# Performance work log

Measured on AMD Instinct MI355X. Metric: run time of the kernel, lower is better.

## Reference

```python
import jax, jax.numpy as jnp
import numpy as np

G, S, P = 128, 32, 16          # graphs, subgraphs per graph, nodes per subgraph
D, C, NH, OUT = 768, 256, 4, 7 # input dim, hidden dim, GAT heads, classes


def setup_inputs() -> dict:
    key = jax.random.key(0)
    ks = jax.random.split(key, 17)
    n = lambda k, shape, s=0.05: jax.random.normal(k, shape, dtype=jnp.float32) * s
    return {
        "x": jax.random.normal(ks[0], (G, S, P, D), dtype=jnp.float32),
        # GATConv(768 -> 256, heads=4, concat=False): lin weight, att vectors, bias
        "gat_W": n(ks[1], (D, NH * C)),
        "att_src": n(ks[2], (NH, C)),
        "att_dst": n(ks[3], (NH, C)),
        "gat_b": n(ks[4], (C,)),
        # GRU(256 -> 256), torch layout [3*H, in]
        "gru_Wih": n(ks[5], (3 * C, C)),
        "gru_Whh": n(ks[6], (3 * C, C)),
        "gru_bih": n(ks[7], (3 * C,)),
        "gru_bhh": n(ks[8], (3 * C,)),
        # scale_up_projection Linear(256 -> 768)
        "up_W": n(ks[9], (D, C)),
        "up_b": n(ks[10], (D,)),
        # speaker_projection Linear(1536 -> 768) + ReLU
        "sp_W": n(ks[11], (D, 2 * D)),
        "sp_b": n(ks[12], (D,)),
        # GlobalAttention gate Linear(256 -> 1)
        "att_W": n(ks[13], (1, C)),
        "att_b": n(ks[14], (1,)),
        # classifier Linear(256 -> 7)
        "cls_W": n(ks[15], (OUT, C)),
        "cls_b": n(ks[16], (OUT,)),
    }


def _gat(x, W, a_src, a_dst, b):
    # PyG GATConv on a star graph (speaker = local node 0 -> all others) with
    # default add_self_loops=True, negative_slope=0.2, concat=False (mean over heads).
    # x: [G, P, D]
    h = jnp.einsum('gpd,dhc->gphc', x, W.reshape(D, NH, C))     # per-head transform
    es = jnp.sum(h * a_src, -1)                                 # [G, P, NH]
    ed = jnp.sum(h * a_dst, -1)
    lrelu = lambda v: jnp.where(v > 0, v, 0.2 * v)
    e_spk = lrelu(es[:, :1] + ed)   # edge speaker -> t
    e_slf = lrelu(es + ed)          # self loop t -> t
    w = jax.nn.softmax(jnp.stack([e_spk, e_slf], -1), axis=-1)  # [G, P, NH, 2]
    # for t == 0 both terms are h[:,0] and weights sum to 1, matching the
    # speaker node receiving only its self loop.
    out = w[..., 0:1] * h[:, :1] + w[..., 1:2] * h              # [G, P, NH, C]
    return out.mean(axis=2) + b


def _gru_cell(xin, h, Wih, Whh, bih, bhh):
    gi = xin @ Wih.T + bih
    gh = h @ Whh.T + bhh
    ir, iz, inn = jnp.split(gi, 3, -1)
    hr, hz, hn = jnp.split(gh, 3, -1)
    r = jax.nn.sigmoid(ir + hr)
    z = jax.nn.sigmoid(iz + hz)
    return (1 - z) * jnp.tanh(inn + r * hn) + z * h


def _forward(x, gat_W, att_src, att_dst, gat_b, gru_Wih, gru_Whh, gru_bih, gru_bhh,
             up_W, up_b, sp_W, sp_b, att_W, att_b, cls_W, cls_b):
    g, s, p, d = x.shape
    m0 = _gat(x[:, 0], gat_W, att_src, att_dst, gat_b)  # [G, P, C]
    h0 = jnp.zeros((g, p, C), x.dtype)

    def step(carry, _):
        h_run, m_prev = carry
        # running GRU hidden over memory prefix, then one zero-input step
        # (equivalent to rerunning the GRU over [m_0..m_{j-1}, 0])
        h_run = _gru_cell(m_prev, h_run, gru_Wih, gru_Whh, gru_bih, gru_bhh)
        h_nxt = _gru_cell(jnp.zeros_like(h_run), h_run, gru_Wih, gru_Whh, gru_bih, gru_bhh)
        pooled = h_nxt @ up_W.T + up_b                  # [G, P, D]
        # faithful to source: non_speaker_indices covers ALL nodes (torch.equal
        # shape-mismatch bug), and speaker_info is read AFTER the overwrite,
        # so the speaker concat is [pooled, pooled] and raw x[:, j>=1] is unused.
        spk = jnp.concatenate([pooled[:, 0], pooled[:, 0]], -1)  # [G, 2D]
        spk = jax.nn.relu(spk @ sp_W.T + sp_b)
        x_new = pooled.at[:, 0].set(spk)
        m = _gat(x_new, gat_W, att_src, att_dst, gat_b)
        return (h_run, m), m

    (_, _), ms = jax.lax.scan(step, (h0, m0), None, length=s - 1)
    mem = jnp.concatenate([m0[None], ms], axis=0)        # [S, G, P, C]
    # GlobalAttention pool over the P nodes of each subgraph memory state
    gate = jax.nn.softmax(jnp.squeeze(mem @ att_W.T + att_b, -1), axis=-1)  # [S, G, P]
    pooled = jnp.einsum('sgp,sgpc->sgc', gate, mem)
    logits = pooled @ cls_W.T + cls_b                    # [S, G, OUT]
    # torch stacks graph-major: [G*S, 1, OUT]
    return jnp.transpose(logits, (1, 0, 2)).reshape(g * s, 1, OUT)


def reference(x, gat_W, att_src, att_dst, gat_b, gru_Wih, gru_Whh, gru_bih, gru_bhh,
              up_W, up_b, sp_W, sp_b, att_W, att_b, cls_W, cls_b):
    return _forward(x, gat_W, att_src, att_dst, gat_b, gru_Wih, gru_Whh, gru_bih,
                    gru_bhh, up_W, up_b, sp_W, sp_b, att_W, att_b, cls_W, cls_b)
```

## Files before the change

### kernel.cpp

```cpp
#include <hip/hip_runtime.h>
#include <math.h>

#define NG 128
#define NS 32
#define NP 16
#define ND 768
#define NC 256
#define NHD 4
#define NOUT 7
#define NR 2048

typedef unsigned short ushortT;
typedef short bf16x8 __attribute__((ext_vector_type(8)));
typedef float f32x4 __attribute__((ext_vector_type(4)));

__device__ __forceinline__ ushortT f2b(float f) {
    union { float f; unsigned u; } v; v.f = f;
    unsigned r = (v.u + 0x7FFF + ((v.u >> 16) & 1)) >> 16;
    return (ushortT)r;
}
__device__ __forceinline__ float b2f(ushortT u) {
    union { unsigned u; float f; } v; v.u = ((unsigned)u) << 16; return v.f;
}
__device__ __forceinline__ float sigf(float v) { return 1.f / (1.f + expf(-v)); }

#define MFMA16(a, b, c) __builtin_amdgcn_mfma_f32_16x16x32_bf16((a), (b), (c), 0, 0, 0)

__global__ __launch_bounds__(512) void gru12spk_kernel(
    const ushortT* __restrict__ mB, const ushortT* __restrict__ hB,
    float* __restrict__ hF,
    const ushortT* __restrict__ WihB, const ushortT* __restrict__ WhhB,
    const ushortT* __restrict__ WusB,
    const float* __restrict__ bih, const float* __restrict__ bhh,
    const float* __restrict__ busv,
    ushortT* __restrict__ hBout, ushortT* __restrict__ hnB,
    ushortT* __restrict__ spkB)
{
    __shared__ short Am[16 * 264];
    __shared__ short Ah[16 * 264];
    __shared__ short Bs[768 * 40];
    const int g = blockIdx.x, tid = threadIdx.x;
    const int w = tid >> 6, lane = tid & 63;
    const int quad = lane >> 4, l15 = lane & 15;
    const int row0 = g * 16;

    {
        const int row = tid >> 5, kc = (tid & 31) * 8;
        *(uint4*)&Am[row * 264 + kc] = *(const uint4*)(mB + (size_t)(row0 + row) * NC + kc);
        *(uint4*)&Ah[row * 264 + kc] = *(const uint4*)(hB + (size_t)(row0 + row) * NC + kc);
    }

    f32x4 ai[3][2], ah[3][2];
#pragma unroll
    for (int gt = 0; gt < 3; ++gt)
#pragma unroll
        for (int nf = 0; nf < 2; ++nf) {
            ai[gt][nf] = (f32x4){0.f, 0.f, 0.f, 0.f};
            ah[gt][nf] = (f32x4){0.f, 0.f, 0.f, 0.f};
        }

    for (int kk = 0; kk < NC; kk += 32) {
        __syncthreads();
        for (int s = tid; s < 3072; s += 512) {
            const int row = s >> 2, kq = (s & 3) * 8;
            *(uint4*)&Bs[row * 40 + kq] = *(const uint4*)(WihB + (size_t)row * NC + kk + kq);
        }
        __syncthreads();
        bf16x8 af = *(const bf16x8*)&Am[l15 * 264 + kk + quad * 8];
#pragma unroll
        for (int gt = 0; gt < 3; ++gt)
#pragma unroll
            for (int nf = 0; nf < 2; ++nf) {
                bf16x8 bv = *(const bf16x8*)&Bs[(gt * 256 + w * 32 + nf * 16 + l15) * 40 + quad * 8];
                ai[gt][nf] = MFMA16(af, bv, ai[gt][nf]);
            }
    }
    for (int kk = 0; kk < NC; kk += 32) {
        __syncthreads();
        for (int s = tid; s < 3072; s += 512) {
            const int row = s >> 2, kq = (s & 3) * 8;
            *(uint4*)&Bs[row * 40 + kq] = *(const uint4*)(WhhB + (size_t)row * NC + kk + kq);
        }
        __syncthreads();
        bf16x8 af = *(const bf16x8*)&Ah[l15 * 264 + kk + quad * 8];
#pragma unroll
        for (int gt = 0; gt < 3; ++gt)
#pragma unroll
            for (int nf = 0; nf < 2; ++nf) {
                bf16x8 bv = *(const bf16x8*)&Bs[(gt * 256 + w * 32 + nf * 16 + l15) * 40 + quad * 8];
                ah[gt][nf] = MFMA16(af, bv, ah[gt][nf]);
            }
    }
    float hreg[2][4];
#pragma unroll
    for (int nf = 0; nf < 2; ++nf) {
        const int c = w * 32 + nf * 16 + l15;
        const float br = bih[c], bz = bih[256 + c], bn = bih[512 + c];
        const float cr = bhh[c], cz = bhh[256 + c], cn = bhh[512 + c];
#pragma unroll
        for (int r = 0; r < 4; ++r) {
            const int row = quad * 4 + r;
            const size_t idx = (size_t)(row0 + row) * NC + c;
            const float hold = hF[idx];
            const float rg = sigf(ai[0][nf][r] + br + ah[0][nf][r] + cr);
            const float zg = sigf(ai[1][nf][r] + bz + ah[1][nf][r] + cz);
            const float ng = tanhf(ai[2][nf][r] + bn + rg * (ah[2][nf][r] + cn));
            const float hn = (1.f - zg) * ng + zg * hold;
            hreg[nf][r] = hn;
            hF[idx] = hn;
            hBout[idx] = f2b(hn);
            Am[row * 264 + c] = (short)f2b(hn);
        }
    }
    f32x4 a2[3][2];
#pragma unroll
    for (int gt = 0; gt < 3; ++gt)
#pragma unroll
        for (int nf = 0; nf < 2; ++nf) a2[gt][nf] = (f32x4){0.f, 0.f, 0.f, 0.f};
    for (int kk = 0; kk < NC; kk += 32) {
        __syncthreads();
        for (int s = tid; s < 3072; s += 512) {
            const int row = s >> 2, kq = (s & 3) * 8;
            *(uint4*)&Bs[row * 40 + kq] = *(const uint4*)(WhhB + (size_t)row * NC + kk + kq);
        }
        __syncthreads();
        bf16x8 af = *(const bf16x8*)&Am[l15 * 264 + kk + quad * 8];
#pragma unroll
        for (int gt = 0; gt < 3; ++gt)
#pragma unroll
            for (int nf = 0; nf < 2; ++nf) {
                bf16x8 bv = *(const bf16x8*)&Bs[(gt * 256 + w * 32 + nf * 16 + l15) * 40 + quad * 8];
                a2[gt][nf] = MFMA16(af, bv, a2[gt][nf]);
            }
    }
#pragma unroll
    for (int nf = 0; nf < 2; ++nf) {
        const int c = w * 32 + nf * 16 + l15;
        const float br = bih[c], bz = bih[256 + c], bn = bih[512 + c];
        const float cr = bhh[c], cz = bhh[256 + c], cn = bhh[512 + c];
#pragma unroll
        for (int r = 0; r < 4; ++r) {
            const int row = quad * 4 + r;
            const size_t idx = (size_t)(row0 + row) * NC + c;
            const float rg = sigf(br + a2[0][nf][r] + cr);
            const float zg = sigf(bz + a2[1][nf][r] + cz);
            const float ng = tanhf(bn + rg * (a2[2][nf][r] + cn));
            const float hv = (1.f - zg) * ng + zg * hreg[nf][r];
            const ushortT hb16 = f2b(hv);
            hnB[idx] = hb16;
            Ah[row * 264 + c] = (short)hb16;
        }
    }
    __syncthreads();
    for (int o = tid; o < ND; o += 512) {
        float s = busv[o];
        const ushortT* wr = WusB + (size_t)o * NC;
#pragma unroll 8
        for (int k8 = 0; k8 < 32; ++k8) {
            bf16x8 hv8 = *(const bf16x8*)&Ah[k8 * 8];
            bf16x8 wv8 = *(const bf16x8*)(wr + k8 * 8);
#pragma unroll
            for (int i = 0; i < 8; ++i) s += b2f((ushortT)hv8[i]) * b2f((ushortT)wv8[i]);
        }
        spkB[(size_t)g * ND + o] = f2b(fmaxf(s, 0.f));
    }
}

__global__ __launch_bounds__(256) void gatovr_kernel(
    const ushortT* __restrict__ hnB, const ushortT* __restrict__ spkB,
    const ushortT* __restrict__ WcombB, const ushortT* __restrict__ gatB,
    const float* __restrict__ bcomb, float* __restrict__ hbuf)
{
    __shared__ short As[64 * 40];
    __shared__ short Bs[64 * 40];
    const int b = blockIdx.x, tid = threadIdx.x;
    const int lane = tid & 63, wid = tid >> 6;
    const int quad = lane >> 4, l15 = lane & 15;
    const int mh = (wid & 1) * 32, nh = (wid >> 1) * 32;
    const int sr = tid >> 2, skq = (tid & 3) * 8;

    const bool ovr = (b >= 512);
    int row0, col0, K;
    const ushortT *A, *Bt;
    if (!ovr) {
        row0 = (b >> 4) * 64; col0 = (b & 15) * 64;
        A = hnB; Bt = WcombB; K = NC;
    } else {
        const int t = b - 512;
        row0 = (t & 1) * 64; col0 = (t >> 1) * 64;
        A = spkB; Bt = gatB; K = ND;
    }
    const ushortT* aptr = A + (size_t)(row0 + sr) * K;
    const ushortT* bptr = Bt + (size_t)(col0 + sr) * K;

    f32x4 acc[2][2];
    for (int i = 0; i < 2; ++i)
        for (int j = 0; j < 2; ++j) acc[i][j] = (f32x4){0.f, 0.f, 0.f, 0.f};

    for (int kk = 0; kk < K; kk += 32) {
        __syncthreads();
        *(uint4*)&As[sr * 40 + skq] = *(const uint4*)(aptr + kk + skq);
        *(uint4*)&Bs[sr * 40 + skq] = *(const uint4*)(bptr + kk + skq);
        __syncthreads();
        bf16x8 af0 = *(const bf16x8*)&As[(mh + l15) * 40 + quad * 8];
        bf16x8 af1 = *(const bf16x8*)&As[(mh + 16 + l15) * 40 + quad * 8];
        bf16x8 bf0 = *(const bf16x8*)&Bs[(nh + l15) * 40 + quad * 8];
        bf16x8 bf1 = *(const bf16x8*)&Bs[(nh + 16 + l15) * 40 + quad * 8];
        acc[0][0] = MFMA16(af0, bf0, acc[0][0]);
        acc[0][1] = MFMA16(af0, bf1, acc[0][1]);
        acc[1][0] = MFMA16(af1, bf0, acc[1][0]);
        acc[1][1] = MFMA16(af1, bf1, acc[1][1]);
    }
#pragma unroll
    for (int mt = 0; mt < 2; ++mt)
#pragma unroll
        for (int nt = 0; nt < 2; ++nt) {
            const int gc = col0 + nh + nt * 16 + l15;
            const float bv = ovr ? 0.f : bcomb[gc];
#pragma unroll
            for (int r = 0; r < 4; ++r) {
                const int gr = row0 + mh + mt * 16 + quad * 4 + r;
                const float v = acc[mt][nt][r] + bv;
                if (ovr) {
                    hbuf[(size_t)(gr * 16) * (NHD * NC) + gc] = v;
                } else if (gr & 15) {
                    hbuf[(size_t)gr * (NHD * NC) + gc] = v;
                }
            }
        }
}

__global__ __launch_bounds__(256) void fin_kernel(
    const float* __restrict__ hbuf, const float* __restrict__ att_src,
    const float* __restrict__ att_dst, const float* __restrict__ gat_b,
    const float* __restrict__ attW, const float* __restrict__ attb,
    const float* __restrict__ clsW, const float* __restrict__ clsb,
    ushortT* __restrict__ mB, float* __restrict__ outp, int s)
{
    const int g = blockIdx.x, tid = threadIdx.x;
    const int lane = tid & 63, wid = tid >> 6;
    __shared__ float es_s[16][4], ed_s[16][4];
    __shared__ float m_s[16][260];
    __shared__ float gate_s[16];
    __shared__ float pooled_s[256];
    const float* hb = hbuf + (size_t)g * NP * (NHD * NC);

    for (int pi = 0; pi < 4; ++pi) {
        const int p = wid * 4 + pi;
        const float* row = hb + p * (NHD * NC);
        float ss[4] = {0.f, 0.f, 0.f, 0.f}, sd[4] = {0.f, 0.f, 0.f, 0.f};
#pragma unroll
        for (int i = 0; i < 16; ++i) {
            const int col = lane + 64 * i;
            const float v = row[col];
            ss[i >> 2] += v * att_src[col];
            sd[i >> 2] += v * att_dst[col];
        }
        for (int off = 32; off; off >>= 1)
#pragma unroll
            for (int h = 0; h < 4; ++h) {
                ss[h] += __shfl_down(ss[h], off);
                sd[h] += __shfl_down(sd[h], off);
            }
        if (lane == 0)
#pragma unroll
            for (int h = 0; h < 4; ++h) { es_s[p][h] = ss[h]; ed_s[p][h] = sd[h]; }
    }
    __syncthreads();
    {
        const int p = tid >> 4, cb = (tid & 15) * 16;
        float accv[16];
#pragma unroll
        for (int cj = 0; cj < 16; ++cj) accv[cj] = 0.f;
#pragma unroll
        for (int h = 0; h < 4; ++h) {
            float e1 = es_s[0][h] + ed_s[p][h]; e1 = e1 > 0.f ? e1 : 0.2f * e1;
            float e2 = es_s[p][h] + ed_s[p][h]; e2 = e2 > 0.f ? e2 : 0.2f * e2;
            const float mx = fmaxf(e1, e2);
            float w0 = expf(e1 - mx), w1 = expf(e2 - mx);
            const float inv = 1.f / (w0 + w1);
            w0 *= inv; w1 *= inv;
            const float* r0 = hb + h * NC + cb;
            const float* rp = hb + p * (NHD * NC) + h * NC + cb;
#pragma unroll
            for (int cj = 0; cj < 16; ++cj) accv[cj] += w0 * r0[cj] + w1 * rp[cj];
        }
#pragma unroll
        for (int cj = 0; cj < 16; ++cj) {
            const float v = accv[cj] * 0.25f + gat_b[cb + cj];
            m_s[p][cb + cj] = v;
            mB[(size_t)(g * NP + p) * NC + cb + cj] = f2b(v);
        }
    }
    __syncthreads();
    for (int pi = 0; pi < 4; ++pi) {
        const int p = wid * 4 + pi;
        float sg = 0.f;
#pragma unroll
        for (int i = 0; i < 4; ++i) { const int c = lane + 64 * i; sg += m_s[p][c] * attW[c]; }
        for (int off = 32; off; off >>= 1) sg += __shfl_down(sg, off);
        if (lane == 0) gate_s[p] = sg + attb[0];
    }
    __syncthreads();
    float mx = -1e30f;
#pragma unroll
    for (int p = 0; p < 16; ++p) mx = fmaxf(mx, gate_s[p]);
    float ge[16], ssum = 0.f;
#pragma unroll
    for (int p = 0; p < 16; ++p) { ge[p] = expf(gate_s[p] - mx); ssum += ge[p]; }
    const float inv = 1.f / ssum;
    {
        float pc = 0.f;
#pragma unroll
        for (int p = 0; p < 16; ++p) pc += ge[p] * m_s[p][tid];
        pooled_s[tid] = pc * inv;
    }
    __syncthreads();
    const int o = tid >> 5, l32 = tid & 31;
    if (o < NOUT) {
        float a = 0.f;
#pragma unroll
        for (int i = 0; i < 8; ++i) {
            const int c = l32 + 32 * i;
            a += pooled_s[c] * clsW[o * NC + c];
        }
        for (int off = 16; off; off >>= 1) a += __shfl_down(a, off);
        if (l32 == 0) outp[((size_t)g * NS + s) * NOUT + o] = a + clsb[o];
    }
}

__global__ __launch_bounds__(256) void bgemm_kernel(
    const ushortT* __restrict__ A, const ushortT* __restrict__ Bt,
    const float* __restrict__ bias, float* __restrict__ outF,
    ushortT* __restrict__ outH, int N, int K, int act)
{
    __shared__ short As[64 * 40];
    __shared__ short Bs[64 * 40];
    const int tid = threadIdx.x;
    const int lane = tid & 63, wid = tid >> 6;
    const int quad = lane >> 4, l15 = lane & 15;
    const int row0 = blockIdx.y * 64, col0 = blockIdx.x * 64;
    const int mh = (wid & 1) * 32, nh = (wid >> 1) * 32;
    const int sr = tid >> 2, skq = (tid & 3) * 8;
    const ushortT* aptr = A + (size_t)(row0 + sr) * K;
    const ushortT* bptr = Bt + (size_t)(col0 + sr) * K;

    f32x4 acc[2][2];
    for (int i = 0; i < 2; ++i)
        for (int j = 0; j < 2; ++j) acc[i][j] = (f32x4){0.f, 0.f, 0.f, 0.f};

    for (int kk = 0; kk < K; kk += 32) {
        __syncthreads();
        *(uint4*)&As[sr * 40 + skq] = *(const uint4*)(aptr + kk + skq);
        *(uint4*)&Bs[sr * 40 + skq] = *(const uint4*)(bptr + kk + skq);
        __syncthreads();
        bf16x8 af0 = *(const bf16x8*)&As[(mh + l15) * 40 + quad * 8];
        bf16x8 af1 = *(const bf16x8*)&As[(mh + 16 + l15) * 40 + quad * 8];
        bf16x8 bf0 = *(const bf16x8*)&Bs[(nh + l15) * 40 + quad * 8];
        bf16x8 bf1 = *(const bf16x8*)&Bs[(nh + 16 + l15) * 40 + quad * 8];
        acc[0][0] = MFMA16(af0, bf0, acc[0][0]);
        acc[0][1] = MFMA16(af0, bf1, acc[0][1]);
        acc[1][0] = MFMA16(af1, bf0, acc[1][0]);
        acc[1][1] = MFMA16(af1, bf1, acc[1][1]);
    }
#pragma unroll
    for (int mt = 0; mt < 2; ++mt)
#pragma unroll
        for (int nt = 0; nt < 2; ++nt) {
            const int gc = col0 + nh + nt * 16 + l15;
            const float bv = bias ? bias[gc] : 0.f;
#pragma unroll
            for (int r = 0; r < 4; ++r) {
                const int gr = row0 + mh + mt * 16 + quad * 4 + r;
                float v = acc[mt][nt][r] + bv;
                if (act) v = fmaxf(v, 0.f);
                if (outF) outF[(size_t)gr * N + gc] = v;
                if (outH) outH[(size_t)gr * N + gc] = f2b(v);
            }
        }
}

__global__ __launch_bounds__(256) void cast_kernel(const float* __restrict__ a,
                                                   ushortT* __restrict__ b, int n) {
    const int i = blockIdx.x * 256 + threadIdx.x;
    if (i < n) b[i] = f2b(a[i]);
}
__global__ __launch_bounds__(256) void gatT_kernel(const float* __restrict__ gW,
                                                   ushortT* __restrict__ gB) {
    const int idx = blockIdx.x * 256 + threadIdx.x;
    const int c = idx / ND, d = idx - c * ND;
    gB[idx] = f2b(gW[(size_t)d * (NHD * NC) + c]);
}
__global__ __launch_bounds__(256) void upwT_kernel(const float* __restrict__ upW,
                                                   ushortT* __restrict__ o) {
    const int idx = blockIdx.x * 256 + threadIdx.x;
    const int k = idx / ND, d = idx - k * ND;
    o[idx] = f2b(upW[(size_t)d * NC + k]);
}
__global__ __launch_bounds__(256) void bcomb_kernel(const float* __restrict__ gW,
                                                    const float* __restrict__ up_b,
                                                    float* __restrict__ bc) {
    const int c = blockIdx.x * 256 + threadIdx.x;
    if (c >= NHD * NC) return;
    float a = 0.f;
    for (int d = 0; d < ND; ++d) a += up_b[d] * gW[(size_t)d * (NHD * NC) + c];
    bc[c] = a;
}
__global__ __launch_bounds__(256) void spwc_kernel(const float* __restrict__ spW,
                                                   float* __restrict__ o) {
    const int idx = blockIdx.x * 256 + threadIdx.x;
    const int r = idx / ND, d = idx - r * ND;
    o[idx] = spW[(size_t)r * (2 * ND) + d] + spW[(size_t)r * (2 * ND) + ND + d];
}
__global__ __launch_bounds__(256) void wus_kernel(const float* __restrict__ spWc,
                                                  const float* __restrict__ upW,
                                                  ushortT* __restrict__ WusB) {
    const int c = threadIdx.x;
    const int o0 = blockIdx.x * 16;
    float acc[16];
#pragma unroll
    for (int i = 0; i < 16; ++i) acc[i] = 0.f;
    for (int d = 0; d < ND; ++d) {
        const float u = upW[(size_t)d * NC + c];
#pragma unroll
        for (int i = 0; i < 16; ++i) acc[i] += spWc[(size_t)(o0 + i) * ND + d] * u;
    }
#pragma unroll
    for (int i = 0; i < 16; ++i) WusB[(size_t)(o0 + i) * NC + c] = f2b(acc[i]);
}
__global__ __launch_bounds__(256) void bus_kernel(const float* __restrict__ spWc,
                                                  const float* __restrict__ up_b,
                                                  const float* __restrict__ sp_b,
                                                  float* __restrict__ bus) {
    const int o = blockIdx.x * 256 + threadIdx.x;
    if (o >= ND) return;
    float a = sp_b[o];
    const float* sr = spWc + (size_t)o * ND;
    for (int d = 0; d < ND; ++d) a += sr[d] * up_b[d];
    bus[o] = a;
}
__global__ __launch_bounds__(256) void x0_kernel(const float* __restrict__ x,
                                                 ushortT* __restrict__ xb) {
    const int idx = blockIdx.x * 256 + threadIdx.x;
    const int row = idx / ND, d = idx - row * ND;
    const int g = row >> 4, p = row & 15;
    xb[idx] = f2b(x[((size_t)g * (NS * NP) + p) * ND + d]);
}
__global__ __launch_bounds__(256) void zh_kernel(float* hF, ushortT* hB) {
    const int idx = blockIdx.x * 256 + threadIdx.x;
    hF[idx] = 0.f;
    hB[idx] = 0;
}

extern "C" void kernel_launch(void* const* d_in, const int* in_sizes, int n_in,
                              void* d_out, int out_size, void* d_ws, size_t ws_size,
                              hipStream_t stream) {
    (void)in_sizes; (void)n_in; (void)out_size; (void)ws_size;
    const float* x       = (const float*)d_in[0];
    const float* gat_W   = (const float*)d_in[1];
    const float* att_src = (const float*)d_in[2];
    const float* att_dst = (const float*)d_in[3];
    const float* gat_b   = (const float*)d_in[4];
    const float* gru_Wih = (const float*)d_in[5];
    const float* gru_Whh = (const float*)d_in[6];
    const float* gru_bih = (const float*)d_in[7];
    const float* gru_bhh = (const float*)d_in[8];
    const float* up_W    = (const float*)d_in[9];
    const float* up_b    = (const float*)d_in[10];
    const float* sp_W    = (const float*)d_in[11];
    const float* sp_b    = (const float*)d_in[12];
    const float* att_W   = (const float*)d_in[13];
    const float* att_b   = (const float*)d_in[14];
    const float* cls_W   = (const float*)d_in[15];
    const float* cls_b   = (const float*)d_in[16];
    float* outp = (float*)d_out;

    char* w = (char*)d_ws;
    ushortT* xb    = (ushortT*)w; w += (size_t)NR * ND * 2;
    ushortT* WihB  = (ushortT*)w; w += (size_t)(3 * NC) * NC * 2;
    ushortT* WhhB  = (ushortT*)w; w += (size_t)(3 * NC) * NC * 2;
    ushortT* gatB  = (ushortT*)w; w += (size_t)(NHD * NC) * ND * 2;
    ushortT* upWT  = (ushortT*)w; w += (size_t)NC * ND * 2;
    ushortT* WcombB= (ushortT*)w; w += (size_t)(NHD * NC) * NC * 2;
    ushortT* WusB  = (ushortT*)w; w += (size_t)ND * NC * 2;
    float*   bcomb = (float*)w;   w += (size_t)(NHD * NC) * 4;
    float*   spWc  = (float*)w;   w += (size_t)ND * ND * 4;
    float*   bus   = (float*)w;   w += (size_t)ND * 4;
    float*   hF    = (float*)w;   w += (size_t)NR * NC * 4;
    ushortT* hB    = (ushortT*)w; w += (size_t)NR * NC * 2;
    ushortT* hnB   = (ushortT*)w; w += (size_t)NR * NC * 2;
    ushortT* spkB  = (ushortT*)w; w += (size_t)NG * ND * 2;
    float*   hbuf  = (float*)w;   w += (size_t)NR * (NHD * NC) * 4;
    ushortT* mB    = (ushortT*)w; w += (size_t)NR * NC * 2;

    cast_kernel<<<768, 256, 0, stream>>>(gru_Wih, WihB, 3 * NC * NC);
    cast_kernel<<<768, 256, 0, stream>>>(gru_Whh, WhhB, 3 * NC * NC);
    gatT_kernel<<<(NHD * NC * ND) / 256, 256, 0, stream>>>(gat_W, gatB);
    upwT_kernel<<<(NC * ND) / 256, 256, 0, stream>>>(up_W, upWT);
    bcomb_kernel<<<(NHD * NC) / 256, 256, 0, stream>>>(gat_W, up_b, bcomb);
    spwc_kernel<<<(ND * ND) / 256, 256, 0, stream>>>(sp_W, spWc);
    wus_kernel<<<ND / 16, 256, 0, stream>>>(spWc, up_W, WusB);
    bus_kernel<<<3, 256, 0, stream>>>(spWc, up_b, sp_b, bus);
    x0_kernel<<<(NR * ND) / 256, 256, 0, stream>>>(x, xb);
    zh_kernel<<<(NR * NC) / 256, 256, 0, stream>>>(hF, hB);
    bgemm_kernel<<<dim3(NC / 64, (NHD * NC) / 64), 256, 0, stream>>>(
        gatB, upWT, nullptr, nullptr, WcombB, NC, ND, 0);

    bgemm_kernel<<<dim3((NHD * NC) / 64, NR / 64), 256, 0, stream>>>(
        xb, gatB, nullptr, hbuf, nullptr, NHD * NC, ND, 0);
    fin_kernel<<<NG, 256, 0, stream>>>(hbuf, att_src, att_dst, gat_b,
                                       att_W, att_b, cls_W, cls_b, mB, outp, 0);

    for (int j = 1; j < NS; ++j) {
        gru12spk_kernel<<<NG, 512, 0, stream>>>(
            mB, hB, hF, WihB, WhhB, WusB, gru_bih, gru_bhh, bus, hB, hnB, spkB);
        gatovr_kernel<<<544, 256, 0, stream>>>(
            hnB, spkB, WcombB, gatB, bcomb, hbuf);
        fin_kernel<<<NG, 256, 0, stream>>>(hbuf, att_src, att_dst, gat_b,
                                           att_W, att_b, cls_W, cls_b, mB, outp, j);
    }
}
```

Measured before the change: 2.958 ms.

## Fuse GAT finalize into GRU step kernel with register-prefetched weight pipeline

Merges the per-step fin_kernel (GAT attention softmax, gate pooling, classifier) into the start of the GRU/speaker kernel, which cuts one launch per recurrence step and keeps the memory state in LDS instead of round-tripping it through global memory. Weight chunks are now double-buffered in registers so the next chunk's global load overlaps the current chunk's MFMAs. The scalar speaker-projection dot product is replaced by MFMA over the same staged pipeline, using only row 0 of the A fragment. Register pressure rises with 12 uint4 prefetch registers, and most of the speaker MFMA work is spent on zero rows.

```diff
diff --git a/kernel.cpp b/kernel.cpp
--- a/kernel.cpp
+++ b/kernel.cpp
@@ -19,35 +19,156 @@
     unsigned r = (v.u + 0x7FFF + ((v.u >> 16) & 1)) >> 16;
     return (ushortT)r;
 }
-__device__ __forceinline__ float b2f(ushortT u) {
-    union { unsigned u; float f; } v; v.u = ((unsigned)u) << 16; return v.f;
-}
 __device__ __forceinline__ float sigf(float v) { return 1.f / (1.f + expf(-v)); }
 
 #define MFMA16(a, b, c) __builtin_amdgcn_mfma_f32_16x16x32_bf16((a), (b), (c), 0, 0, 0)
 
-__global__ __launch_bounds__(512) void gru12spk_kernel(
-    const ushortT* __restrict__ mB, const ushortT* __restrict__ hB,
-    float* __restrict__ hF,
+#define STAGE_CHUNK(c_) do {                                                   \
+    uint4* rb_ = ((c_) & 1) ? rB : rA;                                         \
+    _Pragma("unroll")                                                          \
+    for (int i_ = 0; i_ < 6; ++i_) {                                           \
+        const int slot_ = i_ * 512 + tid;                                      \
+        *(uint4*)&Lb[(slot_ >> 2) * 40 + (slot_ & 3) * 8] = rb_[i_];           \
+    }                                                                          \
+    __syncthreads();                                                           \
+    const int cn_ = (c_) + 2;                                                  \
+    if (cn_ < 32) {                                                            \
+        const ushortT* src_ =                                                  \
+            (cn_ < 8 ? WihB : (cn_ < 24 ? WhhB : WusB)) + (cn_ & 7) * 32;      \
+        _Pragma("unroll")                                                      \
+        for (int i_ = 0; i_ < 6; ++i_) {                                       \
+            const int slot_ = i_ * 512 + tid;                                  \
+            rb_[i_] = *(const uint4*)(src_ + (size_t)(slot_ >> 2) * NC +       \
+                                      (slot_ & 3) * 8);                        \
+        }                                                                      \
+    }                                                                          \
+} while (0)
+
+__global__ __launch_bounds__(512) void stepA_kernel(
+    const float* __restrict__ hbuf, float* __restrict__ hF,
+    ushortT* __restrict__ hB, ushortT* __restrict__ hnB,
+    ushortT* __restrict__ spkB,
     const ushortT* __restrict__ WihB, const ushortT* __restrict__ WhhB,
     const ushortT* __restrict__ WusB,
     const float* __restrict__ bih, const float* __restrict__ bhh,
     const float* __restrict__ busv,
-    ushortT* __restrict__ hBout, ushortT* __restrict__ hnB,
-    ushortT* __restrict__ spkB)
+    const float* __restrict__ att_src, const float* __restrict__ att_dst,
+    const float* __restrict__ gat_b, const float* __restrict__ attW,
+    const float* __restrict__ attb, const float* __restrict__ clsW,
+    const float* __restrict__ clsb, float* __restrict__ outp, int s)
 {
-    __shared__ short Am[16 * 264];
-    __shared__ short Ah[16 * 264];
-    __shared__ short Bs[768 * 40];
+    __shared__ short Lb[768 * 40];
+    __shared__ float m_f[16][264];
+    __shared__ ushortT m_b[16][264];
+    __shared__ ushortT Ahs[16][264];
+    __shared__ float es_s[16][4], ed_s[16][4], gate_s[16], pooled_s[256];
+
     const int g = blockIdx.x, tid = threadIdx.x;
     const int w = tid >> 6, lane = tid & 63;
     const int quad = lane >> 4, l15 = lane & 15;
-    const int row0 = g * 16;
-
+    const int row0g = g * 16;
+    const int ccol0 = w * 32;
+
+    uint4 rA[6], rB[6];
     {
-        const int row = tid >> 5, kc = (tid & 31) * 8;
-        *(uint4*)&Am[row * 264 + kc] = *(const uint4*)(mB + (size_t)(row0 + row) * NC + kc);
-        *(uint4*)&Ah[row * 264 + kc] = *(const uint4*)(hB + (size_t)(row0 + row) * NC + kc);
+        const ushortT* s0 = WihB;
+        const ushortT* s1 = WihB + 32;
+#pragma unroll
+        for (int i = 0; i < 6; ++i) {
+            const int slot = i * 512 + tid, row = slot >> 2, kq = (slot & 3) * 8;
+            rA[i] = *(const uint4*)(s0 + (size_t)row * NC + kq);
+            rB[i] = *(const uint4*)(s1 + (size_t)row * NC + kq);
+        }
+    }
+    {
+        const int row = tid >> 5, kq = (tid & 31) * 8;
+        *(uint4*)&Ahs[row][kq] = *(const uint4*)(hB + (size_t)(row0g + row) * NC + kq);
+    }
+    float hold[2][4];
+#pragma unroll
+    for (int nf = 0; nf < 2; ++nf)
+#pragma unroll
+        for (int r = 0; r < 4; ++r)
+            hold[nf][r] = hF[(size_t)(row0g + quad * 4 + r) * NC + ccol0 + nf * 16 + l15];
+
+    const float* hb = hbuf + (size_t)row0g * (NHD * NC);
+    for (int p = w; p < 16; p += 8) {
+        const float* row = hb + (size_t)p * (NHD * NC);
+        float ss[4] = {0.f, 0.f, 0.f, 0.f}, sd[4] = {0.f, 0.f, 0.f, 0.f};
+#pragma unroll
+        for (int i = 0; i < 16; ++i) {
+            const int col = lane + 64 * i;
+            const float v = row[col];
+            ss[i >> 2] += v * att_src[col];
+            sd[i >> 2] += v * att_dst[col];
+        }
+        for (int off = 32; off; off >>= 1)
+#pragma unroll
+            for (int h = 0; h < 4; ++h) {
+                ss[h] += __shfl_down(ss[h], off);
+                sd[h] += __shfl_down(sd[h], off);
+            }
+        if (lane == 0)
+#pragma unroll
+            for (int h = 0; h < 4; ++h) { es_s[p][h] = ss[h]; ed_s[p][h] = sd[h]; }
+    }
+    __syncthreads();
+    {
+        const int p = tid >> 5, cb = (tid & 31) * 8;
+        float accv[8];
+#pragma unroll
+        for (int cj = 0; cj < 8; ++cj) accv[cj] = 0.f;
+#pragma unroll
+        for (int h = 0; h < 4; ++h) {
+            float e1 = es_s[0][h] + ed_s[p][h]; e1 = e1 > 0.f ? e1 : 0.2f * e1;
+            float e2 = es_s[p][h] + ed_s[p][h]; e2 = e2 > 0.f ? e2 : 0.2f * e2;
+            const float mx = fmaxf(e1, e2);
+            float w0 = expf(e1 - mx), w1 = expf(e2 - mx);
+            const float inv = 1.f / (w0 + w1);
+            w0 *= inv; w1 *= inv;
+            const float* r0 = hb + h * NC + cb;
+            const float* rp = hb + (size_t)p * (NHD * NC) + h * NC + cb;
+#pragma unroll
+            for (int cj = 0; cj < 8; ++cj) accv[cj] += w0 * r0[cj] + w1 * rp[cj];
+        }
+#pragma unroll
+        for (int cj = 0; cj < 8; ++cj) {
+            const float v = accv[cj] * 0.25f + gat_b[cb + cj];
+            m_f[p][cb + cj] = v;
+            m_b[p][cb + cj] = f2b(v);
+        }
+    }
+    __syncthreads();
+    for (int p = w; p < 16; p += 8) {
+        float sg = 0.f;
+#pragma unroll
+        for (int i = 0; i < 4; ++i) { const int c = lane + 64 * i; sg += m_f[p][c] * attW[c]; }
+        for (int off = 32; off; off >>= 1) sg += __shfl_down(sg, off);
+        if (lane == 0) gate_s[p] = sg + attb[0];
+    }
+    __syncthreads();
+    if (tid < 256) {
+        float mx = -1e30f;
+#pragma unroll
+        for (int p = 0; p < 16; ++p) mx = fmaxf(mx, gate_s[p]);
+        float se = 0.f, pc = 0.f;
+#pragma unroll
+        for (int p = 0; p < 16; ++p) {
+            const float e = expf(gate_s[p] - mx);
+            se += e; pc += e * m_f[p][tid];
+        }
+        pooled_s[tid] = pc / se;
+    }
+    __syncthreads();
+    if (w < NOUT) {
+        float a = 0.f;
+#pragma unroll
+        for (int i = 0; i < 4; ++i) {
+            const int c = lane + 64 * i;
+            a += pooled_s[c] * clsW[w * NC + c];
+        }
+        for (int off = 32; off; off >>= 1) a += __shfl_down(a, off);
+        if (lane == 0) outp[((size_t)g * NS + s) * NOUT + w] = a + clsb[w];
     }
 
     f32x4 ai[3][2], ah[3][2];
@@ -58,58 +179,53 @@
             ai[gt][nf] = (f32x4){0.f, 0.f, 0.f, 0.f};
             ah[gt][nf] = (f32x4){0.f, 0.f, 0.f, 0.f};
         }
-
-    for (int kk = 0; kk < NC; kk += 32) {
-        __syncthreads();
-        for (int s = tid; s < 3072; s += 512) {
-            const int row = s >> 2, kq = (s & 3) * 8;
-            *(uint4*)&Bs[row * 40 + kq] = *(const uint4*)(WihB + (size_t)row * NC + kk + kq);
-        }
-        __syncthreads();
-        bf16x8 af = *(const bf16x8*)&Am[l15 * 264 + kk + quad * 8];
+#pragma unroll
+    for (int c = 0; c < 8; ++c) {
+        STAGE_CHUNK(c);
+        const int kk = c * 32;
+        bf16x8 af = *(const bf16x8*)&m_b[l15][kk + quad * 8];
 #pragma unroll
         for (int gt = 0; gt < 3; ++gt)
 #pragma unroll
             for (int nf = 0; nf < 2; ++nf) {
-                bf16x8 bv = *(const bf16x8*)&Bs[(gt * 256 + w * 32 + nf * 16 + l15) * 40 + quad * 8];
+                bf16x8 bv = *(const bf16x8*)&Lb[(gt * 256 + ccol0 + nf * 16 + l15) * 40 + quad * 8];
                 ai[gt][nf] = MFMA16(af, bv, ai[gt][nf]);
             }
-    }
-    for (int kk = 0; kk < NC; kk += 32) {
-        __syncthreads();
-        for (int s = tid; s < 3072; s += 512) {
-            const int row = s >> 2, kq = (s & 3) * 8;
-            *(uint4*)&Bs[row * 40 + kq] = *(const uint4*)(WhhB + (size_t)row * NC + kk + kq);
-        }
-        __syncthreads();
-        bf16x8 af = *(const bf16x8*)&Ah[l15 * 264 + kk + quad * 8];
+        __syncthreads();
+    }
+#pragma unroll
+    for (int c = 8; c < 16; ++c) {
+        STAGE_CHUNK(c);
+        const int kk = (c - 8) * 32;
+        bf16x8 af = *(const bf16x8*)&Ahs[l15][kk + quad * 8];
 #pragma unroll
         for (int gt = 0; gt < 3; ++gt)
 #pragma unroll
             for (int nf = 0; nf < 2; ++nf) {
-                bf16x8 bv = *(const bf16x8*)&Bs[(gt * 256 + w * 32 + nf * 16 + l15) * 40 + quad * 8];
+                bf16x8 bv = *(const bf16x8*)&Lb[(gt * 256 + ccol0 + nf * 16 + l15) * 40 + quad * 8];
                 ah[gt][nf] = MFMA16(af, bv, ah[gt][nf]);
             }
+        __syncthreads();
     }
     float hreg[2][4];
 #pragma unroll
     for (int nf = 0; nf < 2; ++nf) {
-        const int c = w * 32 + nf * 16 + l15;
+        const int c = ccol0 + nf * 16 + l15;
         const float br = bih[c], bz = bih[256 + c], bn = bih[512 + c];
         const float cr = bhh[c], cz = bhh[256 + c], cn = bhh[512 + c];
 #pragma unroll
         for (int r = 0; r < 4; ++r) {
             const int row = quad * 4 + r;
-            const size_t idx = (size_t)(row0 + row) * NC + c;
-            const float hold = hF[idx];
             const float rg = sigf(ai[0][nf][r] + br + ah[0][nf][r] + cr);
             const float zg = sigf(ai[1][nf][r] + bz + ah[1][nf][r] + cz);
             const float ng = tanhf(ai[2][nf][r] + bn + rg * (ah[2][nf][r] + cn));
-            const float hn = (1.f - zg) * ng + zg * hold;
+            const float hn = (1.f - zg) * ng + zg * hold[nf][r];
             hreg[nf][r] = hn;
+            const size_t idx = (size_t)(row0g + row) * NC + c;
             hF[idx] = hn;
-            hBout[idx] = f2b(hn);
-            Am[row * 264 + c] = (short)f2b(hn);
+            const ushortT h16 = f2b(hn);
+            hB[idx] = h16;
+            Ahs[row][c] = h16;
         }
     }
     f32x4 a2[3][2];
@@ -117,52 +233,70 @@
     for (int gt = 0; gt < 3; ++gt)
 #pragma unroll
         for (int nf = 0; nf < 2; ++nf) a2[gt][nf] = (f32x4){0.f, 0.f, 0.f, 0.f};
-    for (int kk = 0; kk < NC; kk += 32) {
-        __syncthreads();
-        for (int s = tid; s < 3072; s += 512) {
-            const int row = s >> 2, kq = (s & 3) * 8;
-            *(uint4*)&Bs[row * 40 + kq] = *(const uint4*)(WhhB + (size_t)row * NC + kk + kq);
-        }
-        __syncthreads();
-        bf16x8 af = *(const bf16x8*)&Am[l15 * 264 + kk + quad * 8];
+#pragma unroll
+    for (int c = 16; c < 24; ++c) {
+        STAGE_CHUNK(c);
+        const int kk = (c - 16) * 32;
+        bf16x8 af = *(const bf16x8*)&Ahs[l15][kk + quad * 8];
 #pragma unroll
         for (int gt = 0; gt < 3; ++gt)
 #pragma unroll
             for (int nf = 0; nf < 2; ++nf) {
-                bf16x8 bv = *(const bf16x8*)&Bs[(gt * 256 + w * 32 + nf * 16 + l15) * 40 + quad * 8];
+                bf16x8 bv = *(const bf16x8*)&Lb[(gt * 256 + ccol0 + nf * 16 + l15) * 40 + quad * 8];
                 a2[gt][nf] = MFMA16(af, bv, a2[gt][nf]);
             }
+        __syncthreads();
     }
 #pragma unroll
     for (int nf = 0; nf < 2; ++nf) {
-        const int c = w * 32 + nf * 16 + l15;
+        const int c = ccol0 + nf * 16 + l15;
         const float br = bih[c], bz = bih[256 + c], bn = bih[512 + c];
         const float cr = bhh[c], cz = bhh[256 + c], cn = bhh[512 + c];
 #pragma unroll
         for (int r = 0; r < 4; ++r) {
             const int row = quad * 4 + r;
-            const size_t idx = (size_t)(row0 + row) * NC + c;
             const float rg = sigf(br + a2[0][nf][r] + cr);
             const float zg = sigf(bz + a2[1][nf][r] + cz);
             const float ng = tanhf(bn + rg * (a2[2][nf][r] + cn));
             const float hv = (1.f - zg) * ng + zg * hreg[nf][r];
-            const ushortT hb16 = f2b(hv);
-            hnB[idx] = hb16;
-            Ah[row * 264 + c] = (short)hb16;
-        }
-    }
-    __syncthreads();
-    for (int o = tid; o < ND; o += 512) {
-        float s = busv[o];
-        const ushortT* wr = WusB + (size_t)o * NC;
-#pragma unroll 8
-        for (int k8 = 0; k8 < 32; ++k8) {
-            bf16x8 hv8 = *(const bf16x8*)&Ah[k8 * 8];
-            bf16x8 wv8 = *(const bf16x8*)(wr + k8 * 8);
-#pragma unroll
-            for (int i = 0; i < 8; ++i) s += b2f((ushortT)hv8[i]) * b2f((ushortT)wv8[i]);
-        }
-        spkB[(size_t)g * ND + o] = f2b(fmaxf(s, 0.f));
+            const ushortT h16 = f2b(hv);
+            hnB[(size_t)(row0g + row) * NC + c] = h16;
+            m_b[row][c] = h16;
+        }
+    }
+    f32x4 aspk[3][2];
+#pragma unroll
+    for (int gt = 0; gt < 3; ++gt)
+#pragma unroll
+        for (int nf = 0; nf < 2; ++nf) aspk[gt][nf] = (f32x4){0.f, 0.f, 0.f, 0.f};
+#pragma unroll
+    for (int c = 24; c < 32; ++c) {
+        STAGE_CHUNK(c);
+        const int kk = (c - 24) * 32;
+        bf16x8 af;
+        if (l15 == 0) {
+            af = *(const bf16x8*)&m_b[0][kk + quad * 8];
+        } else {
+#pragma unroll
+            for (int i = 0; i < 8; ++i) af[i] = 0;
+        }
+#pragma unroll
+        for (int gt = 0; gt < 3; ++gt)
+#pragma unroll
+            for (int nf = 0; nf < 2; ++nf) {
+                bf16x8 bv = *(const bf16x8*)&Lb[(gt * 256 + ccol0 + nf * 16 + l15) * 40 + quad * 8];
+                aspk[gt][nf] = MFMA16(af, bv, aspk[gt][nf]);
+            }
+        __syncthreads();
+    }
+    if (quad == 0) {
+#pragma unroll
+        for (int gt = 0; gt < 3; ++gt)
+#pragma unroll
+            for (int nf = 0; nf < 2; ++nf) {
+                const int col = gt * 256 + ccol0 + nf * 16 + l15;
+                spkB[(size_t)g * ND + col] = f2b(fmaxf(aspk[gt][nf][0] + busv[col], 0.f));
+            }
     }
 }
 
@@ -508,15 +642,15 @@
 
     bgemm_kernel<<<dim3((NHD * NC) / 64, NR / 64), 256, 0, stream>>>(
         xb, gatB, nullptr, hbuf, nullptr, NHD * NC, ND, 0);
-    fin_kernel<<<NG, 256, 0, stream>>>(hbuf, att_src, att_dst, gat_b,
-                                       att_W, att_b, cls_W, cls_b, mB, outp, 0);
 
     for (int j = 1; j < NS; ++j) {
-        gru12spk_kernel<<<NG, 512, 0, stream>>>(
-            mB, hB, hF, WihB, WhhB, WusB, gru_bih, gru_bhh, bus, hB, hnB, spkB);
+        stepA_kernel<<<NG, 512, 0, stream>>>(
+            hbuf, hF, hB, hnB, spkB, WihB, WhhB, WusB,
+            gru_bih, gru_bhh, bus, att_src, att_dst, gat_b,
+            att_W, att_b, cls_W, cls_b, outp, j - 1);
         gatovr_kernel<<<544, 256, 0, stream>>>(
             hnB, spkB, WcombB, gatB, bcomb, hbuf);
-        fin_kernel<<<NG, 256, 0, stream>>>(hbuf, att_src, att_dst, gat_b,
-                                           att_W, att_b, cls_W, cls_b, mB, outp, j);
-    }
-}
+    }
+    fin_kernel<<<NG, 256, 0, stream>>>(hbuf, att_src, att_dst, gat_b,
+                                       att_W, att_b, cls_W, cls_b, mB, outp, 31);
+}
```

Result: slower. 3.851 ms (+30.2%).
